# Optimization experiments

Measured on AMD Instinct MI355X. Metric: run time of the kernel, lower is better.

Reference implementation:

```python
import jax, jax.numpy as jnp
import numpy as np

B, S, D = 4, 2048, 1024
E = 8
DFF = 4096
CAP_FACTOR = 1.25


def setup_inputs() -> dict:
    key = jax.random.key(0)
    ks = jax.random.split(key, 4)
    std_gate = float(np.sqrt(0.1 / D))
    inputs = jax.random.normal(ks[0], (B, S, D), dtype=jnp.float32)
    gate_w = jax.random.normal(ks[1], (E, D), dtype=jnp.float32) * std_gate
    w1 = jax.random.normal(ks[2], (E, D, DFF), dtype=jnp.float32) * (1.0 / np.sqrt(D))
    b1 = jnp.zeros((E, DFF), dtype=jnp.float32)
    w2 = jax.random.normal(ks[3], (E, DFF, D), dtype=jnp.float32) * (1.0 / np.sqrt(DFF))
    b2 = jnp.zeros((E, D), dtype=jnp.float32)
    return {"inputs": inputs, "gate_w": gate_w, "w1": w1, "b1": b1, "w2": w2, "b2": b2}


def reference(inputs, gate_w, w1, b1, w2, b2):
    d_model = inputs.shape[-1]
    tokens = inputs.reshape(-1, d_model)            # [T, D]
    T = tokens.shape[0]
    num_experts = gate_w.shape[0]
    capacity = int(np.ceil(CAP_FACTOR * T / num_experts))

    # fp32 gate (FP32LinearGate): logits = tokens @ gate_w.T
    logits = jnp.einsum('td,ed->te', tokens.astype(jnp.float32), gate_w)
    probs = jax.nn.softmax(logits, axis=-1)         # [T, E]

    # Top-1 routing with capacity
    expert_idx = jnp.argmax(probs, axis=-1)         # [T]
    mask = jax.nn.one_hot(expert_idx, num_experts, dtype=jnp.float32)  # [T, E]
    ranks = jnp.cumsum(mask, axis=0) - 1.0          # position of each token within its expert
    keep = (ranks < capacity) * mask                # drop tokens over capacity, [T, E]
    pos = ranks.astype(jnp.int32)                   # [T, E]
    # sec_mask: [T, E, C] one-hot placement of kept tokens into capacity slots
    sec_mask = jax.nn.one_hot(pos, capacity, dtype=jnp.float32) * keep[:, :, None]
    combine_weights = probs[:, :, None] * sec_mask  # [T, E, C]

    # Dispatch: dense matmul against routing mask (fallback path of MoeLayer)
    dispatch = jnp.einsum('tec,td->ecd', sec_mask, tokens)  # [E, C, D]

    # Grouped expert FFN
    h = jax.nn.relu(jnp.einsum('ecd,edh->ech', dispatch, w1) + b1[:, None, :])
    expert_out = jnp.einsum('ech,ehd->ecd', h, w2) + b2[:, None, :]  # [E, C, D]

    # Combine
    ans = jnp.einsum('tec,ecd->td', combine_weights, expert_out)
    return ans.reshape(inputs.shape)
```

## Files before the change

kernel.cpp:

```cpp
#include <hip/hip_runtime.h>
#include <hip/hip_bf16.h>

#define TOKENS 8192
#define DMODEL 1024
#define NEXP   8
#define DFF    4096
#define CAP    1280

typedef short bf16x8_t __attribute__((ext_vector_type(8)));
typedef float f32x4_t  __attribute__((ext_vector_type(4)));

__device__ __forceinline__ float bf2f(ushort u) {
    union { unsigned int i; float f; } v; v.i = ((unsigned int)u) << 16; return v.f;
}
__device__ __forceinline__ ushort f2bf(float f) {
    union { float f; unsigned int i; } v; v.f = f;
    unsigned int r = v.i + 0x7fffu + ((v.i >> 16) & 1u);
    return (ushort)(r >> 16);
}
__device__ __forceinline__ void load_lds16(const void* g, void* l) {
    __builtin_amdgcn_global_load_lds(
        (const __attribute__((address_space(1))) void*)g,
        (__attribute__((address_space(3))) void*)l, 16, 0, 0);
}

__global__ __launch_bounds__(256) void gate_kernel(
    const float* __restrict__ tokens, const float* __restrict__ gw,
    int* __restrict__ eidx, float* __restrict__ prob)
{
    int lane = threadIdx.x & 63;
    int wave = threadIdx.x >> 6;
    int t = blockIdx.x * 4 + wave;
    const float* tok = tokens + (long)t * DMODEL;
    float s[NEXP] = {0.f,0.f,0.f,0.f,0.f,0.f,0.f,0.f};
    #pragma unroll
    for (int c = 0; c < 4; c++) {
        int d = c * 256 + lane * 4;
        float4 x = *(const float4*)(tok + d);
        #pragma unroll
        for (int e = 0; e < NEXP; e++) {
            float4 g = *(const float4*)(gw + e * DMODEL + d);
            s[e] += x.x*g.x + x.y*g.y + x.z*g.z + x.w*g.w;
        }
    }
    #pragma unroll
    for (int e = 0; e < NEXP; e++) {
        #pragma unroll
        for (int off = 32; off > 0; off >>= 1) s[e] += __shfl_xor(s[e], off);
    }
    if (lane == 0) {
        float m = s[0]; int am = 0;
        #pragma unroll
        for (int e = 1; e < NEXP; e++) if (s[e] > m) { m = s[e]; am = e; }
        float sum = 0.f;
        #pragma unroll
        for (int e = 0; e < NEXP; e++) sum += expf(s[e] - m);
        eidx[t] = am;
        prob[t] = 1.0f / sum;
    }
}

__global__ __launch_bounds__(1024) void route_scan(
    const int* __restrict__ eidx, int* __restrict__ pos, int* __restrict__ cnt)
{
    __shared__ unsigned long long pa[16], pb[16];
    int tid = threadIdx.x;
    int lane = tid & 63, wid = tid >> 6;
    int4 e0 = *(const int4*)(eidx + tid * 8);
    int4 e1 = *(const int4*)(eidx + tid * 8 + 4);
    int le[8] = {e0.x, e0.y, e0.z, e0.w, e1.x, e1.y, e1.z, e1.w};
    unsigned long long ha = 0, hb = 0;
    #pragma unroll
    for (int i = 0; i < 8; i++) {
        int e = le[i];
        if (e < 4) ha += 1ull << (e * 16);
        else       hb += 1ull << ((e - 4) * 16);
    }
    unsigned long long ia = ha, ib = hb;
    #pragma unroll
    for (int off = 1; off < 64; off <<= 1) {
        unsigned long long ua = __shfl_up(ia, off);
        unsigned long long ub = __shfl_up(ib, off);
        if (lane >= off) { ia += ua; ib += ub; }
    }
    if (lane == 63) { pa[wid] = ia; pb[wid] = ib; }
    __syncthreads();
    if (tid < 64) {
        unsigned long long va = (lane < 16) ? pa[lane] : 0;
        unsigned long long vb = (lane < 16) ? pb[lane] : 0;
        unsigned long long oa = va, ob = vb;
        #pragma unroll
        for (int off = 1; off < 16; off <<= 1) {
            unsigned long long ua = __shfl_up(va, off);
            unsigned long long ub = __shfl_up(vb, off);
            if (lane >= off) { va += ua; vb += ub; }
        }
        if (lane < 16) { pa[lane] = va - oa; pb[lane] = vb - ob; }
        if (lane == 15) {
            #pragma unroll
            for (int e = 0; e < 4; e++) {
                cnt[e]     = (int)((va >> (e * 16)) & 0xffffu);
                cnt[e + 4] = (int)((vb >> (e * 16)) & 0xffffu);
            }
        }
    }
    __syncthreads();
    unsigned long long ba = pa[wid] + (ia - ha);
    unsigned long long bb = pb[wid] + (ib - hb);
    int po[8];
    #pragma unroll
    for (int i = 0; i < 8; i++) {
        int e = le[i];
        if (e < 4) { int sh = e * 16;       po[i] = (int)((ba >> sh) & 0xffffu); ba += 1ull << sh; }
        else       { int sh = (e - 4) * 16; po[i] = (int)((bb >> sh) & 0xffffu); bb += 1ull << sh; }
    }
    *(int4*)(pos + tid * 8)     = (int4){po[0], po[1], po[2], po[3]};
    *(int4*)(pos + tid * 8 + 4) = (int4){po[4], po[5], po[6], po[7]};
}

__global__ __launch_bounds__(256) void dispatch_gather(
    const float* __restrict__ tokens, const int* __restrict__ eidx,
    const int* __restrict__ pos, ushort* __restrict__ disp)
{
    int t = blockIdx.x;
    int p = pos[t];
    if (p >= CAP) return;
    int e = eidx[t];
    int d = threadIdx.x * 4;
    float4 v = *(const float4*)(tokens + (long)t * DMODEL + d);
    union { uint2 u; ushort h[4]; } o;
    o.h[0] = f2bf(v.x); o.h[1] = f2bf(v.y); o.h[2] = f2bf(v.z); o.h[3] = f2bf(v.w);
    *(uint2*)(disp + ((long)e * CAP + p) * DMODEL + d) = o.u;
}

__global__ __launch_bounds__(256) void transpose_f32_bf16(
    const float* __restrict__ in, ushort* __restrict__ out, int R, int C)
{
    __shared__ ushort tile[64 * 64];
    long base = (long)blockIdx.z * R * C;
    int r0 = blockIdx.y * 64, c0 = blockIdx.x * 64;
    int tid = threadIdx.x;
    int rr = tid >> 4;
    int cf = (tid & 15) * 4;
    const float* ip = in + base + (long)(r0 + rr) * C + c0 + cf;
    #pragma unroll
    for (int q = 0; q < 4; q++) {
        int r = rr + q * 16;
        float4 v = *(const float4*)(ip + (long)q * 16 * C);
        int rlo = r & 7, rhi = r >> 3;
        tile[(cf+0) * 64 + ((rhi ^ ((cf+0) & 7)) << 3) + rlo] = f2bf(v.x);
        tile[(cf+1) * 64 + ((rhi ^ ((cf+1) & 7)) << 3) + rlo] = f2bf(v.y);
        tile[(cf+2) * 64 + ((rhi ^ ((cf+2) & 7)) << 3) + rlo] = f2bf(v.z);
        tile[(cf+3) * 64 + ((rhi ^ ((cf+3) & 7)) << 3) + rlo] = f2bf(v.w);
    }
    __syncthreads();
    int oc = tid >> 3;
    int j  = tid & 7;
    #pragma unroll
    for (int q = 0; q < 2; q++) {
        int c = oc + q * 32;
        uint4 w = *(const uint4*)&tile[c * 64 + ((j ^ (c & 7)) << 3)];
        *(uint4*)(out + base + (long)(c0 + c) * R + r0 + j * 8) = w;
    }
}

__global__ __launch_bounds__(256) void gemm_bt(
    const ushort* __restrict__ A, const ushort* __restrict__ B,
    const float* __restrict__ bias, ushort* __restrict__ C,
    const int* __restrict__ cnt,
    int M, int N, int K, int do_relu,
    long sA, long sB, long sBias, long sC)
{
    if ((int)blockIdx.y * 128 >= cnt[blockIdx.z]) return;

    A += blockIdx.z * sA; B += blockIdx.z * sB;
    bias += blockIdx.z * sBias; C += blockIdx.z * sC;

    __shared__ ushort As[128 * 64];
    __shared__ ushort Bs[128 * 64];

    int tid  = threadIdx.x;
    int lane = tid & 63, wave = tid >> 6;
    int wm = (wave >> 1) * 64, wn = (wave & 1) * 64;
    int fm = lane & 15;
    int q  = lane >> 4;
    int rx = fm & 7;
    int m0 = blockIdx.y * 128, n0 = blockIdx.x * 128;

    int srow = lane >> 3;
    int schk = (lane & 7) ^ srow;
    const ushort* Ag = A + (long)(m0 + 32*wave + srow) * K + schk * 8;
    const ushort* Bg = B + (long)(n0 + 32*wave + srow) * K + schk * 8;
    ushort* AsW = &As[(32*wave) * 64];
    ushort* BsW = &Bs[(32*wave) * 64];

    f32x4_t acc[4][4];
    #pragma unroll
    for (int i = 0; i < 4; i++)
        #pragma unroll
        for (int j = 0; j < 4; j++) acc[i][j] = (f32x4_t){0.f,0.f,0.f,0.f};

    for (int k0 = 0; k0 < K; k0 += 64) {
        #pragma unroll
        for (int t = 0; t < 4; t++) {
            load_lds16(Ag + (long)(8*t) * K + k0, AsW + (8*t) * 64);
            load_lds16(Bg + (long)(8*t) * K + k0, BsW + (8*t) * 64);
        }
        __syncthreads();
        #pragma unroll
        for (int kk = 0; kk < 64; kk += 32) {
            int l0 = (kk >> 3) + q;
            bf16x8_t af[4], bf[4];
            #pragma unroll
            for (int i = 0; i < 4; i++) {
                int r = wm + 16*i + fm;
                af[i] = *(const bf16x8_t*)&As[r * 64 + (l0 ^ rx) * 8];
            }
            #pragma unroll
            for (int j = 0; j < 4; j++) {
                int r = wn + 16*j + fm;
                bf[j] = *(const bf16x8_t*)&Bs[r * 64 + (l0 ^ rx) * 8];
            }
            #pragma unroll
            for (int i = 0; i < 4; i++)
                #pragma unroll
                for (int j = 0; j < 4; j++)
                    acc[i][j] = __builtin_amdgcn_mfma_f32_16x16x32_bf16(af[i], bf[j], acc[i][j], 0, 0, 0);
        }
        __syncthreads();
    }

    #pragma unroll
    for (int j = 0; j < 4; j++) {
        int col = n0 + wn + 16*j + fm;
        float bv = bias[col];
        #pragma unroll
        for (int i = 0; i < 4; i++) {
            int row = m0 + wm + 16*i + q * 4;
            #pragma unroll
            for (int r = 0; r < 4; r++) {
                float v = acc[i][j][r] + bv;
                if (do_relu) v = fmaxf(v, 0.f);
                C[(long)(row + r) * N + col] = f2bf(v);
            }
        }
    }
}

__global__ __launch_bounds__(256) void combine_kernel(
    const ushort* __restrict__ eo, const int* __restrict__ eidx,
    const int* __restrict__ pos, const float* __restrict__ prob,
    float* __restrict__ out)
{
    int t = blockIdx.x;
    int p = pos[t];
    int d = threadIdx.x * 4;
    float4 o;
    if (p < CAP) {
        int e = eidx[t];
        float w = prob[t];
        union { uint2 u; ushort h[4]; } v;
        v.u = *(const uint2*)(eo + ((long)e * CAP + p) * DMODEL + d);
        o.x = w * bf2f(v.h[0]);
        o.y = w * bf2f(v.h[1]);
        o.z = w * bf2f(v.h[2]);
        o.w = w * bf2f(v.h[3]);
    } else {
        o = (float4){0.f, 0.f, 0.f, 0.f};
    }
    *(float4*)(out + (long)t * DMODEL + d) = o;
}

extern "C" void kernel_launch(void* const* d_in, const int* in_sizes, int n_in,
                              void* d_out, int out_size, void* d_ws, size_t ws_size,
                              hipStream_t stream) {
    const float* tokens = (const float*)d_in[0];
    const float* gate_w = (const float*)d_in[1];
    const float* w1     = (const float*)d_in[2];
    const float* b1     = (const float*)d_in[3];
    const float* w2     = (const float*)d_in[4];
    const float* b2     = (const float*)d_in[5];
    float* outp = (float*)d_out;

    char* w = (char*)d_ws;
    ushort* w1T  = (ushort*)w; w += (size_t)NEXP * DFF * DMODEL * 2;
    ushort* w2T  = (ushort*)w; w += (size_t)NEXP * DMODEL * DFF * 2;
    ushort* disp = (ushort*)w; w += (size_t)NEXP * CAP * DMODEL * 2;
    ushort* h    = (ushort*)w; w += (size_t)NEXP * CAP * DFF * 2;
    ushort* eo   = (ushort*)w; w += (size_t)NEXP * CAP * DMODEL * 2;
    int*   eidx  = (int*)w;   w += TOKENS * 4;
    int*   pos   = (int*)w;   w += TOKENS * 4;
    float* prob  = (float*)w; w += TOKENS * 4;
    int*   cnt   = (int*)w;   w += NEXP * 4;

    transpose_f32_bf16<<<dim3(DFF/64, DMODEL/64, NEXP), 256, 0, stream>>>(w1, w1T, DMODEL, DFF);
    transpose_f32_bf16<<<dim3(DMODEL/64, DFF/64, NEXP), 256, 0, stream>>>(w2, w2T, DFF, DMODEL);

    gate_kernel<<<TOKENS/4, 256, 0, stream>>>(tokens, gate_w, eidx, prob);
    route_scan<<<1, 1024, 0, stream>>>(eidx, pos, cnt);
    dispatch_gather<<<TOKENS, 256, 0, stream>>>(tokens, eidx, pos, disp);

    gemm_bt<<<dim3(DFF/128, CAP/128, NEXP), 256, 0, stream>>>(
        disp, w1T, b1, h, cnt, CAP, DFF, DMODEL, 1,
        (long)CAP*DMODEL, (long)DFF*DMODEL, DFF, (long)CAP*DFF);
    gemm_bt<<<dim3(DMODEL/128, CAP/128, NEXP), 256, 0, stream>>>(
        h, w2T, b2, eo, cnt, CAP, DMODEL, DFF, 0,
        (long)CAP*DFF, (long)DMODEL*DFF, DMODEL, (long)CAP*DMODEL);

    combine_kernel<<<TOKENS, 256, 0, stream>>>(eo, eidx, pos, prob, outp);
}
```

Measured before the change: 563.2 us.

## Replace first expert GEMM with 256x256-tile, 4-stage pipelined 8-wave kernel

Adds a new grouped GEMM for the first expert FFN layer. It uses 256x256 output tiles, 512 threads, a four-slot LDS ring fed by direct global-to-LDS loads, XOR-swizzled LDS, and s_setprio around MFMA bursts. Workgroup IDs are swizzled across groups of eight to improve cache locality. The goal is to raise MFMA utilisation and hide memory latency. In exchange, the larger tiles mean fewer workgroups, coarser capacity skipping at 256-row granularity, and more register pressure.

```diff
diff --git a/kernel.cpp b/kernel.cpp
--- a/kernel.cpp
+++ b/kernel.cpp
@@ -162,6 +162,131 @@
         uint4 w = *(const uint4*)&tile[c * 64 + ((j ^ (c & 7)) << 3)];
         *(uint4*)(out + base + (long)(c0 + c) * R + r0 + j * 8) = w;
     }
+}
+
+__global__ __launch_bounds__(512, 2) void gemm1_8ph(
+    const ushort* __restrict__ A, const ushort* __restrict__ B,
+    const float* __restrict__ bias, ushort* __restrict__ C,
+    const int* __restrict__ cnt,
+    int N, int K, int do_relu,
+    long sA, long sB, long sBias, long sC)
+{
+    __shared__ ushort As[4 * 8192];
+    __shared__ ushort Bs[4 * 8192];
+
+    int gx = gridDim.x, gy = gridDim.y;
+    int nwg = gx * gy * gridDim.z;
+    int lin = blockIdx.x + gx * (blockIdx.y + gy * blockIdx.z);
+    int cpx = nwg >> 3;
+    int swz = (lin & 7) * cpx + (lin >> 3);
+    int bz  = swz / (gx * gy);
+    int rem = swz - bz * gx * gy;
+    int by  = rem / gx, bx = rem - by * gx;
+
+    if (by * 256 >= cnt[bz]) return;
+
+    A += bz * sA; B += bz * sB; bias += bz * sBias; C += bz * sC;
+    long m0 = (long)by * 256, n0 = (long)bx * 256;
+
+    int tid  = threadIdx.x;
+    int lane = tid & 63, wave = tid >> 6;
+    int wm = (wave >> 2) * 128;
+    int wn = (wave & 3) * 64;
+    int fm = lane & 15;
+    int q  = lane >> 4;
+    int rxk = (q ^ ((fm >> 1) & 3)) * 8;
+
+    int tr0 = tid >> 2, tr1 = tr0 + 128;
+    int pc  = tid & 3;
+    int lc0 = pc ^ ((tr0 >> 1) & 3);
+    int lc1 = pc ^ ((tr1 >> 1) & 3);
+    const ushort* AgS0 = A + (long)(m0 + tr0) * K + lc0 * 8;
+    const ushort* AgS1 = A + (long)(m0 + tr1) * K + lc1 * 8;
+    const ushort* BgS0 = B + (long)(n0 + tr0) * K + lc0 * 8;
+    const ushort* BgS1 = B + (long)(n0 + tr1) * K + lc1 * 8;
+    int wb = wave * 512;
+
+#define STAGE_A(s, ko) do { \
+    load_lds16(AgS0 + (ko), &As[(s) * 8192 + wb]); \
+    load_lds16(AgS1 + (ko), &As[(s) * 8192 + 4096 + wb]); } while (0)
+#define STAGE_B(s, ko) do { \
+    load_lds16(BgS0 + (ko), &Bs[(s) * 8192 + wb]); \
+    load_lds16(BgS1 + (ko), &Bs[(s) * 8192 + 4096 + wb]); } while (0)
+
+    f32x4_t acc[8][4];
+    #pragma unroll
+    for (int i = 0; i < 8; i++)
+        #pragma unroll
+        for (int j = 0; j < 4; j++) acc[i][j] = (f32x4_t){0.f,0.f,0.f,0.f};
+
+    int KT = K >> 6;
+
+    STAGE_B(0, 0);  STAGE_A(0, 0);
+    STAGE_B(1, 32); STAGE_A(1, 32);
+    STAGE_B(2, 64); STAGE_A(2, 64);
+    STAGE_B(3, 96);
+    asm volatile("s_waitcnt vmcnt(6)" ::: "memory");
+    __builtin_amdgcn_s_barrier();
+
+    bf16x8_t bfr[4];
+    for (int kt = 0; kt < KT; ++kt) {
+        #pragma unroll
+        for (int p = 0; p < 4; ++p) {
+            const int ch = p & 1, kh = p >> 1;
+            const int sl = ((kt << 1) + kh) & 3;
+            const ushort* Asl = &As[sl * 8192];
+            const ushort* Bsl = &Bs[sl * 8192];
+            if (ch == 0) {
+                #pragma unroll
+                for (int j = 0; j < 4; j++) {
+                    int r = wn + 16*j + fm;
+                    bfr[j] = *(const bf16x8_t*)&Bsl[r * 32 + rxk];
+                }
+            }
+            bf16x8_t af[4];
+            #pragma unroll
+            for (int i = 0; i < 4; i++) {
+                int r = wm + ch*64 + 16*i + fm;
+                af[i] = *(const bf16x8_t*)&Asl[r * 32 + rxk];
+            }
+            if (p == 0)      { if (kt+1 < KT) STAGE_A((((kt+1)<<1)+1)&3, (kt+1)*64 + 32); }
+            else if (p == 1) { if (kt+2 < KT) STAGE_B(( (kt+2)<<1     )&3, (kt+2)*64     ); }
+            else if (p == 2) { if (kt+2 < KT) STAGE_A(( (kt+2)<<1     )&3, (kt+2)*64     ); }
+            else             { if (kt+2 < KT) STAGE_B((((kt+2)<<1)+1)&3, (kt+2)*64 + 32); }
+            __builtin_amdgcn_s_barrier();
+            __builtin_amdgcn_s_setprio(1);
+            #pragma unroll
+            for (int i = 0; i < 4; i++)
+                #pragma unroll
+                for (int j = 0; j < 4; j++)
+                    acc[ch*4 + i][j] = __builtin_amdgcn_mfma_f32_16x16x32_bf16(
+                        af[i], bfr[j], acc[ch*4 + i][j], 0, 0, 0);
+            __builtin_amdgcn_s_setprio(0);
+            if (p == 3) {
+                if (kt < KT - 2) asm volatile("s_waitcnt vmcnt(6)" ::: "memory");
+                else             asm volatile("s_waitcnt vmcnt(0)" ::: "memory");
+            }
+            __builtin_amdgcn_s_barrier();
+        }
+    }
+
+    #pragma unroll
+    for (int j = 0; j < 4; j++) {
+        long col = n0 + wn + 16*j + fm;
+        float bv = bias[col];
+        #pragma unroll
+        for (int i = 0; i < 8; i++) {
+            long row = m0 + wm + 16*i + q * 4;
+            #pragma unroll
+            for (int r = 0; r < 4; r++) {
+                float v = acc[i][j][r] + bv;
+                if (do_relu) v = fmaxf(v, 0.f);
+                C[(row + r) * N + col] = f2bf(v);
+            }
+        }
+    }
+#undef STAGE_A
+#undef STAGE_B
 }
 
 __global__ __launch_bounds__(256) void gemm_bt(
@@ -300,8 +425,8 @@
     route_scan<<<1, 1024, 0, stream>>>(eidx, pos, cnt);
     dispatch_gather<<<TOKENS, 256, 0, stream>>>(tokens, eidx, pos, disp);
 
-    gemm_bt<<<dim3(DFF/128, CAP/128, NEXP), 256, 0, stream>>>(
-        disp, w1T, b1, h, cnt, CAP, DFF, DMODEL, 1,
+    gemm1_8ph<<<dim3(DFF/256, CAP/256, NEXP), 512, 0, stream>>>(
+        disp, w1T, b1, h, cnt, DFF, DMODEL, 1,
         (long)CAP*DMODEL, (long)DFF*DMODEL, DFF, (long)CAP*DFF);
     gemm_bt<<<dim3(DMODEL/128, CAP/128, NEXP), 256, 0, stream>>>(
         h, w2T, b2, eo, cnt, CAP, DMODEL, DFF, 0,
```

Measured after the change: 587.4 us. 4.3% more time.
